# Kernel tuning notes

Measured on AMD Instinct MI355X. Metric: run time of the kernel, lower is better.

## Reference

```python
import jax, jax.numpy as jnp
import numpy as np

MIN_NORM = 1e-15
PROJ_EPS = 4e-3


def _artanh(x):
    x = jnp.clip(x, -1 + 1e-7, 1 - 1e-7)
    return 0.5 * (jnp.log1p(x) - jnp.log1p(-x))


def _norm(x):
    return jnp.clip(jnp.linalg.norm(x, axis=-1, keepdims=True), MIN_NORM)


def proj(x, c):
    norm = _norm(x)
    maxnorm = (1.0 - PROJ_EPS) / jnp.sqrt(c)
    return jnp.where(norm > maxnorm, x / norm * maxnorm, x)


def expmap0(u, c):
    sqrt_c = jnp.sqrt(c)
    u_norm = _norm(u)
    return jnp.tanh(sqrt_c * u_norm) * u / (sqrt_c * u_norm)


def logmap0(p, c):
    sqrt_c = jnp.sqrt(c)
    p_norm = _norm(p)
    return _artanh(sqrt_c * p_norm) * p / (sqrt_c * p_norm)


def mobius_add(x, y, c):
    x2 = jnp.sum(x * x, axis=-1, keepdims=True)
    y2 = jnp.sum(y * y, axis=-1, keepdims=True)
    xy = jnp.sum(x * y, axis=-1, keepdims=True)
    num = (1 + 2 * c * xy + c * y2) * x + (1 - c * x2) * y
    denom = 1 + 2 * c * xy + c * c * x2 * y2
    return num / jnp.clip(denom, MIN_NORM)


def mobius_matvec(m, x, c):
    sqrt_c = jnp.sqrt(c)
    x_norm = _norm(x)
    mx = x @ m.T
    mx_norm = _norm(mx)
    res = jnp.tanh(mx_norm / x_norm * _artanh(sqrt_c * x_norm)) * mx / (mx_norm * sqrt_c)
    zero_row = jnp.all(mx == 0, axis=-1, keepdims=True)
    return jnp.where(zero_row, jnp.zeros_like(res), res)


def setup_inputs() -> dict:
    key = jax.random.key(0)
    k1, k2, k3, k4, k5 = jax.random.split(key, 5)
    n, d, e = 50000, 128, 800000
    c = jnp.float32(1.0)
    x = 0.1 * jax.random.normal(k1, (n, d), dtype=jnp.float32)
    x = proj(x, c)  # points on the Poincare ball
    adj = jax.random.randint(k2, (2, e), 0, n, dtype=jnp.int64)
    w = jax.random.uniform(k3, (e,), dtype=jnp.float32)
    weight = jax.random.normal(k4, (d, d), dtype=jnp.float32) * (1.0 / np.sqrt(d))
    bias = jax.random.normal(k5, (d,), dtype=jnp.float32) * 0.01
    return {"x": x, "adj": adj, "w": w, "weight": weight, "bias": bias}


def reference(x, adj, w, weight, bias):
    c_in = jnp.float32(1.0)
    c_out = jnp.float32(1.0)
    n = x.shape[0]

    # HypLinear (dropout p=0 -> identity on weight)
    mv = mobius_matvec(weight, x, c_in)
    res = proj(mv, c_in)
    b = bias.reshape(1, -1)  # proj_tan0 is identity on the Poincare ball
    hyp_bias = proj(expmap0(b, c_in), c_in)
    h = proj(mobius_add(res, hyp_bias, c_in), c_in)

    # HypAgg: logmap0 -> weighted segment_sum over edges -> expmap0 -> proj
    s, r = adj[0], adj[1]
    ht = logmap0(h, c_in)
    x_s = ht[s] * w[:, None]  # [E, d]
    x_agg = jax.ops.segment_sum(x_s, r, num_segments=n)
    h = proj(expmap0(x_agg, c_in), c_in)

    # HypAct: act(logmap0) -> expmap0 -> proj
    xt = jax.nn.relu(logmap0(h, c_in))
    out = proj(expmap0(xt, c_out), c_out)
    return (out, adj)
```

## Files before the change

### kernel.cpp

```cpp
#include <hip/hip_runtime.h>
#include <math.h>

#define MAXN 0.996f
#define MINN 1e-15f
#define CAP  5120

typedef __bf16   bf16x8  __attribute__((ext_vector_type(8)));
typedef _Float16 halfx8  __attribute__((ext_vector_type(8)));
typedef _Float16 half2_t __attribute__((ext_vector_type(2)));
typedef float    floatx4 __attribute__((ext_vector_type(4)));

__device__ __forceinline__ float wsum(float v){
  v += __shfl_xor(v, 32);
  v += __shfl_xor(v, 16);
  v += __shfl_xor(v, 8);
  v += __shfl_xor(v, 4);
  v += __shfl_xor(v, 2);
  v += __shfl_xor(v, 1);
  return v;
}

__device__ __forceinline__ float artanh_(float v){
  v = fminf(fmaxf(v, -1.f + 1e-7f), 1.f - 1e-7f);
  return 0.5f * (log1pf(v) - log1pf(-v));
}

__device__ __forceinline__ int block_excl_scan(int v, int tid, int* wsums){
  int lane = tid & 63, wid = tid >> 6;
  int iv = v;
#pragma unroll
  for(int o = 1; o < 64; o <<= 1){
    int t = __shfl_up(iv, o);
    if(lane >= o) iv += t;
  }
  if(lane == 63) wsums[wid] = iv;
  __syncthreads();
  int wbase = 0;
  for(int k = 0; k < wid; k++) wbase += wsums[k];
  return wbase + iv - v;
}

__global__ __launch_bounds__(256)
void fusedA_kernel(const float* __restrict__ x, const float* __restrict__ W,
                   const float* __restrict__ bias, _Float16* __restrict__ ht, int n,
                   const int* __restrict__ adj, const float* __restrict__ w,
                   float* __restrict__ adj_out, int* __restrict__ bucketSize,
                   int2* __restrict__ part, int E, int nA)
{
  __shared__ __align__(16) char smem[43264];
  const int tid = threadIdx.x;

  if(blockIdx.x < nA){
    int* hist  = (int*)smem;
    int* wcur  = (int*)(smem + 4096);
    int* lbase = (int*)(smem + 8192);
    int* gbase = (int*)(smem + 9216);
    int* wsA   = (int*)(smem + 10240);
    int2* stag = (int2*)(smem + 10256);

    const int wv = tid >> 6;
#pragma unroll
    for(int k = 0; k < 4; k++) hist[k*256 + tid] = 0;
    __syncthreads();

    const int e0 = blockIdx.x * 4096;
    int p0r[16], p1r[16];
#pragma unroll
    for(int k = 0; k < 16; k++){
      int e = e0 + k*256 + tid;
      if(e < E){
        int s = adj[e];
        int r = adj[e + E];
        float we = w[e];
        adj_out[e]     = (float)s;
        adj_out[e + E] = (float)r;
        int b = r >> 8;
        p0r[k] = s | ((r & 255) << 16) | (b << 24);
        p1r[k] = __float_as_int(we);
        atomicAdd(&hist[wv*256 + b], 1);
      }
    }
    __syncthreads();
    int h0 = hist[0*256+tid], h1 = hist[1*256+tid], h2 = hist[2*256+tid], h3 = hist[3*256+tid];
    int cb = h0 + h1 + h2 + h3;
    int lb = block_excl_scan(cb, tid, wsA);
    lbase[tid]      = lb;
    wcur[0*256+tid] = lb;
    wcur[1*256+tid] = lb + h0;
    wcur[2*256+tid] = lb + h0 + h1;
    wcur[3*256+tid] = lb + h0 + h1 + h2;
    gbase[tid] = cb ? atomicAdd(&bucketSize[tid], cb) : 0;
    __syncthreads();
#pragma unroll
    for(int k = 0; k < 16; k++){
      int e = e0 + k*256 + tid;
      if(e < E){
        int b = ((unsigned)p0r[k]) >> 24;
        int pos = atomicAdd(&wcur[wv*256 + b], 1);
        stag[pos] = make_int2(p0r[k], p1r[k]);
      }
    }
    __syncthreads();
    int total = (e0 + 4096 <= E) ? 4096 : (E - e0);
    for(int i = tid; i < total; i += 256){
      int2 p = stag[i];
      int b = ((unsigned)p.x) >> 24;
      int loc = gbase[b] + (i - lbase[b]);
      if(loc < CAP) part[(size_t)b * CAP + loc] = p;
    }
    return;
  }

  __bf16* Wh   = (__bf16*)smem;
  float* hb_sh = (float*)(smem + 32768);
  float* y2_sh = (float*)(smem + 33280);

  for(int g = tid; g < 2048; g += 256){
    int nr = g >> 4, k16 = g & 15;
    const float* wp = W + nr * 128 + k16 * 8;
    float4 a = *(const float4*)wp;
    float4 b = *(const float4*)(wp + 4);
    bf16x8 h;
    h[0]=(__bf16)a.x; h[1]=(__bf16)a.y; h[2]=(__bf16)a.z; h[3]=(__bf16)a.w;
    h[4]=(__bf16)b.x; h[5]=(__bf16)b.y; h[6]=(__bf16)b.z; h[7]=(__bf16)b.w;
    *(bf16x8*)&Wh[nr * 128 + ((k16 ^ (nr & 15)) << 3)] = h;
  }
  if(tid < 64){
    int l = tid;
    float b0 = bias[l], b1 = bias[l + 64];
    float bn = fmaxf(sqrtf(wsum(b0*b0 + b1*b1)), MINN);
    float sb = tanhf(bn) / bn;
    float hb0 = sb*b0, hb1 = sb*b1;
    float hnn = fmaxf(sqrtf(wsum(hb0*hb0 + hb1*hb1)), MINN);
    if(hnn > MAXN){ float f = MAXN/hnn; hb0 *= f; hb1 *= f; }
    float y2 = wsum(hb0*hb0 + hb1*hb1);
    hb_sh[l] = hb0; hb_sh[l + 64] = hb1;
    if(l == 0) *y2_sh = y2;
  }
  __syncthreads();

  const int lane = tid & 63;
  const int wid  = tid >> 6;
  const int q    = lane >> 4;
  const int n15  = lane & 15;

  const int M0 = (blockIdx.x - nA) * 64 + wid * 16;
  if(M0 >= n) return;

  float hbv[8];
#pragma unroll
  for(int t = 0; t < 8; t++) hbv[t] = hb_sh[t*16 + n15];
  const float y2 = *y2_sh;

  floatx4 acc[8];
#pragma unroll
  for(int t = 0; t < 8; t++) acc[t] = (floatx4){0.f,0.f,0.f,0.f};

  float x2p = 0.f;
  int m = M0 + n15; if(m > n - 1) m = n - 1;
#pragma unroll
  for(int kk = 0; kk < 4; kk++){
    const float* xp = x + (size_t)m * 128 + kk * 32 + q * 8;
    float4 xa = *(const float4*)xp;
    float4 xb = *(const float4*)(xp + 4);
    x2p += xa.x*xa.x + xa.y*xa.y + xa.z*xa.z + xa.w*xa.w
         + xb.x*xb.x + xb.y*xb.y + xb.z*xb.z + xb.w*xb.w;
    bf16x8 a;
    a[0]=(__bf16)xa.x; a[1]=(__bf16)xa.y; a[2]=(__bf16)xa.z; a[3]=(__bf16)xa.w;
    a[4]=(__bf16)xb.x; a[5]=(__bf16)xb.y; a[6]=(__bf16)xb.z; a[7]=(__bf16)xb.w;
    int k16 = kk * 4 + q;
#pragma unroll
    for(int t = 0; t < 8; t++){
      bf16x8 b = *(bf16x8*)&Wh[(t*16 + n15) * 128 + ((k16 ^ n15) << 3)];
      acc[t] = __builtin_amdgcn_mfma_f32_16x16x32_bf16(a, b, acc[t], 0, 0, 0);
    }
  }
  x2p += __shfl_xor(x2p, 16);
  x2p += __shfl_xor(x2p, 32);

  float mp[4], dp[4];
#pragma unroll
  for(int i = 0; i < 4; i++){
    float mpi = 0.f, dpi = 0.f;
#pragma unroll
    for(int t = 0; t < 8; t++){ float v = acc[t][i]; mpi = fmaf(v, v, mpi); dpi = fmaf(v, hbv[t], dpi); }
    mpi += __shfl_xor(mpi, 1); mpi += __shfl_xor(mpi, 2); mpi += __shfl_xor(mpi, 4); mpi += __shfl_xor(mpi, 8);
    dpi += __shfl_xor(dpi, 1); dpi += __shfl_xor(dpi, 2); dpi += __shfl_xor(dpi, 4); dpi += __shfl_xor(dpi, 8);
    mp[i] = mpi; dp[i] = dpi;
  }

  const int li   = lane & 3;
  const int srcl = (((lane >> 2) << 4) | li) & 63;
  float selmp = li==0 ? mp[0] : li==1 ? mp[1] : li==2 ? mp[2] : mp[3];
  float seldp = li==0 ? dp[0] : li==1 ? dp[1] : li==2 ? dp[2] : dp[3];
  float tmp_mp = __shfl(selmp, srcl);
  float tmp_dp = __shfl(seldp, srcl);
  float mxn = fmaxf(sqrtf(tmp_mp), MINN);
  float xn  = fmaxf(sqrtf(x2p), MINN);
  float tt  = tanhf(mxn / xn * artanh_(xn));
  float s1  = tt / mxn;
  float rn  = fmaxf(tt, MINN);
  if(rn > MAXN) s1 *= MAXN / rn;
  float xy    = s1 * tmp_dp;
  float r2    = s1 * s1 * tmp_mp;
  float alpha = 1.f + 2.f*xy + y2;
  float beta  = 1.f - r2;
  float inv   = 1.f / fmaxf(1.f + 2.f*xy + r2*y2, MINN);
  float as1   = alpha * s1;

  float as1b[4], betab[4], invb[4];
#pragma unroll
  for(int i = 0; i < 4; i++){
    int sl = ((lane >> 4) << 2) | i;
    as1b[i]  = __shfl(as1, sl);
    betab[i] = __shfl(beta, sl);
    invb[i]  = __shfl(inv, sl);
  }

  float uv[4][8];
  float u2[4];
#pragma unroll
  for(int i = 0; i < 4; i++){
    float u2i = 0.f;
#pragma unroll
    for(int t = 0; t < 8; t++){
      float u = (as1b[i] * acc[t][i] + betab[i] * hbv[t]) * invb[i];
      uv[i][t] = u;
      u2i = fmaf(u, u, u2i);
    }
    u2i += __shfl_xor(u2i, 1); u2i += __shfl_xor(u2i, 2); u2i += __shfl_xor(u2i, 4); u2i += __shfl_xor(u2i, 8);
    u2[i] = u2i;
  }

  float selu = li==0 ? u2[0] : li==1 ? u2[1] : li==2 ? u2[2] : u2[3];
  float tu   = __shfl(selu, srcl);
  float un = fmaxf(sqrtf(tu), MINN);
  float sc = 1.f, hn = un;
  if(un > MAXN){ sc = MAXN/un; hn = MAXN; }
  float lt = artanh_(hn) / hn * sc;

#pragma unroll
  for(int i = 0; i < 4; i++){
    int grow = M0 + q * 4 + i;
    float lti = __shfl(lt, ((lane >> 4) << 2) | i);
    if(grow < n){
      halfx8 f;
#pragma unroll
      for(int t = 0; t < 8; t++) f[t] = (_Float16)(lti * uv[i][t]);
      *(halfx8*)(ht + (size_t)grow * 128 + n15 * 8) = f;
    }
  }
}

__global__ __launch_bounds__(256)
void passB_kernel(const int* __restrict__ bucketSize, const int2* __restrict__ part,
                  unsigned* __restrict__ epk, int* __restrict__ offs, int n)
{
  __shared__ int sizes[256];
  __shared__ int hist[256];
  __shared__ int cursor[256];
  __shared__ int wsA[4];
  __shared__ int2 stag[CAP];

  const int tid = threadIdx.x;
  const int b   = blockIdx.x;
  sizes[tid] = bucketSize[tid];
  hist[tid]  = 0;
  __syncthreads();
  int sb = block_excl_scan(sizes[tid], tid, wsA);
  __shared__ int base_sh;
  if(tid == b) base_sh = sb;
  __syncthreads();
  const int base_b = base_sh;
  int size = sizes[b]; if(size > CAP) size = CAP;

  const int2* src = part + (size_t)b * CAP;
  for(int i = tid; i < size; i += 256){
    int2 p = src[i];
    stag[i] = p;
    atomicAdd(&hist[(((unsigned)p.x) >> 16) & 255], 1);
  }
  __syncthreads();
  int rb = block_excl_scan(hist[tid], tid, wsA);
  int grow = b * 256 + tid;
  if(grow <= n) offs[grow] = base_b + rb;
  cursor[tid] = rb;
  __syncthreads();
  for(int i = tid; i < size; i += 256){
    int2 p = stag[i];
    int rlo = (((unsigned)p.x) >> 16) & 255;
    int pos = atomicAdd(&cursor[rlo], 1);
    unsigned wh = (unsigned)__builtin_bit_cast(unsigned short,
                    (_Float16)__builtin_bit_cast(float, p.y));
    epk[base_b + pos] = (unsigned)(p.x & 0xFFFF) | (wh << 16);
  }
}

__global__ __launch_bounds__(256)
void agg_act_kernel(const int* __restrict__ offs, const unsigned* __restrict__ epk,
                    const _Float16* __restrict__ ht, float* __restrict__ out, int n)
{
  __shared__ float tr[4][4][132];
  const int tid  = threadIdx.x;
  const int wid  = tid >> 6;
  const int lane = tid & 63;
  const int g = lane >> 4, i = lane & 15;
  const int row = blockIdx.x * 16 + wid * 4 + g;
  const char* htb = (const char*)ht;
  const int ioff = i << 4;

  half2_t acc2[4];
#pragma unroll
  for(int k = 0; k < 4; k++) acc2[k] = (half2_t){(_Float16)0.f, (_Float16)0.f};

#define EDGE(pk) { \
    int s_ = (int)((pk) & 0xFFFFu); \
    half2_t w2_ = __builtin_bit_cast(half2_t, __builtin_amdgcn_perm(pk, pk, 0x03020302u)); \
    int4 q_ = *(const int4*)(htb + ((s_ << 8) | ioff)); \
    acc2[0] = __builtin_bit_cast(half2_t, q_.x) * w2_ + acc2[0]; \
    acc2[1] = __builtin_bit_cast(half2_t, q_.y) * w2_ + acc2[1]; \
    acc2[2] = __builtin_bit_cast(half2_t, q_.z) * w2_ + acc2[2]; \
    acc2[3] = __builtin_bit_cast(half2_t, q_.w) * w2_ + acc2[3]; \
  }

  if(row < n){
    int beg = offs[row];
    int m   = offs[row + 1] - beg;
    const unsigned* ep = epk + beg;
    int t = 0;
    for(; t + 1 < m; t += 2){
      unsigned pk0 = ep[t];
      unsigned pk1 = ep[t + 1];
      EDGE(pk0);
      EDGE(pk1);
    }
    if(t < m) EDGE(ep[t]);
  }
#undef EDGE

  float acc[8];
#pragma unroll
  for(int k = 0; k < 4; k++){
    acc[2*k]   = (float)acc2[k][0];
    acc[2*k+1] = (float)acc2[k][1];
  }
  float u2p = 0.f;
#pragma unroll
  for(int k = 0; k < 8; k++) u2p = fmaf(acc[k], acc[k], u2p);
  u2p += __shfl_xor(u2p, 1); u2p += __shfl_xor(u2p, 2);
  u2p += __shfl_xor(u2p, 4); u2p += __shfl_xor(u2p, 8);
  float un = fmaxf(sqrtf(u2p), MINN);
  float te = tanhf(un);
  float se = te / un;
  float gn = fmaxf(te, MINN);
  float hn = gn;
  if(gn > MAXN){ se *= MAXN/gn; hn = MAXN; }
  float la = artanh_(hn) / hn * se;
  float l[8];
  float r2p = 0.f;
#pragma unroll
  for(int k = 0; k < 8; k++){ l[k] = fmaxf(la*acc[k], 0.f); r2p = fmaf(l[k], l[k], r2p); }
  r2p += __shfl_xor(r2p, 1); r2p += __shfl_xor(r2p, 2);
  r2p += __shfl_xor(r2p, 4); r2p += __shfl_xor(r2p, 8);
  float rn = fmaxf(sqrtf(r2p), MINN);
  float t2 = tanhf(rn);
  float s2 = t2 / rn;
  float on = fmaxf(t2, MINN);
  if(on > MAXN) s2 *= MAXN/on;

  if(row < n){
#pragma unroll
    for(int k = 0; k < 8; k++) tr[wid][g][k*16 + i] = s2 * l[k];
    float4 o0 = *(float4*)&tr[wid][g][i*8];
    float4 o1 = *(float4*)&tr[wid][g][i*8 + 4];
    float* orow = out + (size_t)row * 128 + i*8;
    *(float4*)orow       = o0;
    *(float4*)(orow + 4) = o1;
  }
}

extern "C" void kernel_launch(void* const* d_in, const int* in_sizes, int n_in,
                              void* d_out, int out_size, void* d_ws, size_t ws_size,
                              hipStream_t stream)
{
  const float* x    = (const float*)d_in[0];
  const int*   adj  = (const int*)  d_in[1];
  const float* w    = (const float*)d_in[2];
  const float* W    = (const float*)d_in[3];
  const float* bias = (const float*)d_in[4];
  const int n = in_sizes[0] / 128;
  const int E = in_sizes[2];

  float* out     = (float*)d_out;
  float* adj_out = out + (size_t)n * 128;

  char* ws = (char*)d_ws;
  _Float16* ht   = (_Float16*)ws;  ws += (size_t)n * 128 * sizeof(_Float16);
  int2*  part    = (int2*)ws;      ws += (size_t)256 * CAP * sizeof(int2);
  unsigned* epk  = (unsigned*)ws;  ws += (size_t)E * sizeof(unsigned);
  int*   offs    = (int*)ws;       ws += (size_t)(n + 1) * sizeof(int);
  int*   bucketSize = (int*)ws;

  const int nA = (E + 4095) / 4096;
  const int nS = (n + 63) / 64;

  hipMemsetAsync(bucketSize, 0, 256 * sizeof(int), stream);
  fusedA_kernel<<<nA + nS, 256, 0, stream>>>(x, W, bias, ht, n,
                                             adj, w, adj_out, bucketSize, part, E, nA);
  passB_kernel<<<(n + 255) / 256, 256, 0, stream>>>(bucketSize, part, epk, offs, n);
  agg_act_kernel<<<(n + 15) / 16, 256, 0, stream>>>(offs, epk, ht, out, n);
}
```

Baseline: 153.8 us.

## Halve partition chunk size, prefetch x rows early, unroll gather by four

The partition blocks now handle 2048 edges instead of 4096, which shrinks shared memory (33 KB instead of 43 KB) and doubles the number of partition blocks, so more blocks can be resident at once. The matvec blocks issue their x row loads before converting W to bf16 in shared memory, so load latency overlaps the conversion. The aggregation loop now issues four independent gathers before accumulating, which exposes more memory-level parallelism. The cost is more global atomics on the bucket counters and higher register pressure in the gather loop.

```diff
diff --git a/kernel.cpp b/kernel.cpp
--- a/kernel.cpp
+++ b/kernel.cpp
@@ -47,7 +47,7 @@
                    float* __restrict__ adj_out, int* __restrict__ bucketSize,
                    int2* __restrict__ part, int E, int nA)
 {
-  __shared__ __align__(16) char smem[43264];
+  __shared__ __align__(16) char smem[33296];
   const int tid = threadIdx.x;
 
   if(blockIdx.x < nA){
@@ -63,10 +63,10 @@
     for(int k = 0; k < 4; k++) hist[k*256 + tid] = 0;
     __syncthreads();
 
-    const int e0 = blockIdx.x * 4096;
-    int p0r[16], p1r[16];
-#pragma unroll
-    for(int k = 0; k < 16; k++){
+    const int e0 = blockIdx.x * 2048;
+    int p0r[8], p1r[8];
+#pragma unroll
+    for(int k = 0; k < 8; k++){
       int e = e0 + k*256 + tid;
       if(e < E){
         int s = adj[e];
@@ -92,7 +92,7 @@
     gbase[tid] = cb ? atomicAdd(&bucketSize[tid], cb) : 0;
     __syncthreads();
 #pragma unroll
-    for(int k = 0; k < 16; k++){
+    for(int k = 0; k < 8; k++){
       int e = e0 + k*256 + tid;
       if(e < E){
         int b = ((unsigned)p0r[k]) >> 24;
@@ -101,7 +101,7 @@
       }
     }
     __syncthreads();
-    int total = (e0 + 4096 <= E) ? 4096 : (E - e0);
+    int total = (e0 + 2048 <= E) ? 2048 : (E - e0);
     for(int i = tid; i < total; i += 256){
       int2 p = stag[i];
       int b = ((unsigned)p.x) >> 24;
@@ -114,6 +114,23 @@
   __bf16* Wh   = (__bf16*)smem;
   float* hb_sh = (float*)(smem + 32768);
   float* y2_sh = (float*)(smem + 33280);
+
+  const int lane = tid & 63;
+  const int wid  = tid >> 6;
+  const int q    = lane >> 4;
+  const int n15  = lane & 15;
+  const int M0   = (blockIdx.x - nA) * 64 + wid * 16;
+
+  float4 xa[4], xb[4];
+  {
+    int m = M0 + n15; if(m > n - 1) m = n - 1; if(m < 0) m = 0;
+    const float* xr = x + (size_t)m * 128 + q * 8;
+#pragma unroll
+    for(int kk = 0; kk < 4; kk++){
+      xa[kk] = *(const float4*)(xr + kk * 32);
+      xb[kk] = *(const float4*)(xr + kk * 32 + 4);
+    }
+  }
 
   for(int g = tid; g < 2048; g += 256){
     int nr = g >> 4, k16 = g & 15;
@@ -139,12 +156,6 @@
   }
   __syncthreads();
 
-  const int lane = tid & 63;
-  const int wid  = tid >> 6;
-  const int q    = lane >> 4;
-  const int n15  = lane & 15;
-
-  const int M0 = (blockIdx.x - nA) * 64 + wid * 16;
   if(M0 >= n) return;
 
   float hbv[8];
@@ -157,17 +168,14 @@
   for(int t = 0; t < 8; t++) acc[t] = (floatx4){0.f,0.f,0.f,0.f};
 
   float x2p = 0.f;
-  int m = M0 + n15; if(m > n - 1) m = n - 1;
 #pragma unroll
   for(int kk = 0; kk < 4; kk++){
-    const float* xp = x + (size_t)m * 128 + kk * 32 + q * 8;
-    float4 xa = *(const float4*)xp;
-    float4 xb = *(const float4*)(xp + 4);
-    x2p += xa.x*xa.x + xa.y*xa.y + xa.z*xa.z + xa.w*xa.w
-         + xb.x*xb.x + xb.y*xb.y + xb.z*xb.z + xb.w*xb.w;
+    float4 a4 = xa[kk], b4 = xb[kk];
+    x2p += a4.x*a4.x + a4.y*a4.y + a4.z*a4.z + a4.w*a4.w
+         + b4.x*b4.x + b4.y*b4.y + b4.z*b4.z + b4.w*b4.w;
     bf16x8 a;
-    a[0]=(__bf16)xa.x; a[1]=(__bf16)xa.y; a[2]=(__bf16)xa.z; a[3]=(__bf16)xa.w;
-    a[4]=(__bf16)xb.x; a[5]=(__bf16)xb.y; a[6]=(__bf16)xb.z; a[7]=(__bf16)xb.w;
+    a[0]=(__bf16)a4.x; a[1]=(__bf16)a4.y; a[2]=(__bf16)a4.z; a[3]=(__bf16)a4.w;
+    a[4]=(__bf16)b4.x; a[5]=(__bf16)b4.y; a[6]=(__bf16)b4.z; a[7]=(__bf16)b4.w;
     int k16 = kk * 4 + q;
 #pragma unroll
     for(int t = 0; t < 8; t++){
@@ -313,14 +321,12 @@
 #pragma unroll
   for(int k = 0; k < 4; k++) acc2[k] = (half2_t){(_Float16)0.f, (_Float16)0.f};
 
-#define EDGE(pk) { \
-    int s_ = (int)((pk) & 0xFFFFu); \
-    half2_t w2_ = __builtin_bit_cast(half2_t, __builtin_amdgcn_perm(pk, pk, 0x03020302u)); \
-    int4 q_ = *(const int4*)(htb + ((s_ << 8) | ioff)); \
-    acc2[0] = __builtin_bit_cast(half2_t, q_.x) * w2_ + acc2[0]; \
-    acc2[1] = __builtin_bit_cast(half2_t, q_.y) * w2_ + acc2[1]; \
-    acc2[2] = __builtin_bit_cast(half2_t, q_.z) * w2_ + acc2[2]; \
-    acc2[3] = __builtin_bit_cast(half2_t, q_.w) * w2_ + acc2[3]; \
+#define WDUP(pk) __builtin_bit_cast(half2_t, __builtin_amdgcn_perm(pk, pk, 0x03020302u))
+#define ACCUM(qv, w2) { \
+    acc2[0] = __builtin_bit_cast(half2_t, (qv).x) * (w2) + acc2[0]; \
+    acc2[1] = __builtin_bit_cast(half2_t, (qv).y) * (w2) + acc2[1]; \
+    acc2[2] = __builtin_bit_cast(half2_t, (qv).z) * (w2) + acc2[2]; \
+    acc2[3] = __builtin_bit_cast(half2_t, (qv).w) * (w2) + acc2[3]; \
   }
 
   if(row < n){
@@ -328,15 +334,24 @@
     int m   = offs[row + 1] - beg;
     const unsigned* ep = epk + beg;
     int t = 0;
-    for(; t + 1 < m; t += 2){
-      unsigned pk0 = ep[t];
-      unsigned pk1 = ep[t + 1];
-      EDGE(pk0);
-      EDGE(pk1);
-    }
-    if(t < m) EDGE(ep[t]);
-  }
-#undef EDGE
+    for(; t + 3 < m; t += 4){
+      unsigned pka = ep[t], pkb = ep[t+1], pkc = ep[t+2], pkd = ep[t+3];
+      const int4 qa = *(const int4*)(htb + ((int)(pka & 0xFFFFu) << 8 | ioff));
+      const int4 qb = *(const int4*)(htb + ((int)(pkb & 0xFFFFu) << 8 | ioff));
+      const int4 qc = *(const int4*)(htb + ((int)(pkc & 0xFFFFu) << 8 | ioff));
+      const int4 qd = *(const int4*)(htb + ((int)(pkd & 0xFFFFu) << 8 | ioff));
+      half2_t wa = WDUP(pka), wb = WDUP(pkb), wc = WDUP(pkc), wd = WDUP(pkd);
+      ACCUM(qa, wa); ACCUM(qb, wb); ACCUM(qc, wc); ACCUM(qd, wd);
+    }
+    for(; t < m; t++){
+      unsigned pk = ep[t];
+      const int4 q_ = *(const int4*)(htb + ((int)(pk & 0xFFFFu) << 8 | ioff));
+      half2_t w2 = WDUP(pk);
+      ACCUM(q_, w2);
+    }
+  }
+#undef ACCUM
+#undef WDUP
 
   float acc[8];
 #pragma unroll
@@ -401,7 +416,7 @@
   int*   offs    = (int*)ws;       ws += (size_t)(n + 1) * sizeof(int);
   int*   bucketSize = (int*)ws;
 
-  const int nA = (E + 4095) / 4096;
+  const int nA = (E + 2047) / 2048;
   const int nS = (n + 63) / 64;
 
   hipMemsetAsync(bucketSize, 0, 256 * sizeof(int), stream);
```

After: 156.7 us. About the same (+1.9%).
